# Optimization experiments

Hardware: AMD Instinct MI355X
Metric: run time of the kernel (lower is better)

## Reference

```python
import jax, jax.numpy as jnp
import numpy as np

STATE_DIM = 32
OBS_DIM = 16
PROCESS_VAR = 1e-4
MEAS_VAR = 1e-2
B = 2048
T = 64


def setup_inputs() -> dict:
    key = jax.random.key(0)
    k1, k2, k3 = jax.random.split(key, 3)
    state0 = jax.random.normal(k1, (B, STATE_DIM), dtype=jnp.float32)
    # Initial covariance P = I (per torch __init__), broadcast over batch
    cov0 = jnp.broadcast_to(jnp.eye(STATE_DIM, dtype=jnp.float32), (B, STATE_DIM, STATE_DIM))
    measurements = jax.random.normal(k2, (B, T, OBS_DIM), dtype=jnp.float32)
    # Parameters per torch __init__: F = eye, H = randn, Q = pv*I, R = mv*I
    F = jnp.eye(STATE_DIM, dtype=jnp.float32)
    H = jax.random.normal(k3, (OBS_DIM, STATE_DIM), dtype=jnp.float32)
    Q = PROCESS_VAR * jnp.eye(STATE_DIM, dtype=jnp.float32)
    R = MEAS_VAR * jnp.eye(OBS_DIM, dtype=jnp.float32)
    return {"state0": state0, "cov0": cov0, "measurements": measurements,
            "F": F, "H": H, "Q": Q, "R": R}


def reference(state0, cov0, measurements, F, H, Q, R):
    """Run Kalman predict+update over T timesteps; return filtered states (B,T,S)."""

    def step(carry, z):
        x, P = carry  # x: (B,S), P: (B,S,S); z: (B,O)
        # --- predict ---
        x_pred = x @ F.T                                   # F @ x per batch
        P_pred = jnp.einsum('ij,bjk,lk->bil', F, P, F) + Q  # F P F^T + Q
        # --- update ---
        y = x_pred @ H.T                                   # predicted measurement (B,O)
        innov = z - y
        S = jnp.einsum('ij,bjk,lk->bil', H, P_pred, H) + R  # (B,O,O)
        S_inv = jnp.linalg.inv(S)
        K = jnp.einsum('bij,kj,bkl->bil', P_pred, H, S_inv)  # P H^T S^{-1}, (B,S,O)
        x_new = x_pred + jnp.einsum('bij,bj->bi', K, innov)
        P_new = P_pred - jnp.einsum('bij,jk,bkl->bil', K, H, P_pred)  # (I - K H) P
        return (x_new, P_new), x_new

    # scan over time axis: measurements (B,T,O) -> (T,B,O)
    (_, _), states = jax.lax.scan(step, (state0, cov0), jnp.swapaxes(measurements, 0, 1))
    return jnp.swapaxes(states, 0, 1)  # (B,T,S)
```

## Files before the change

kernel.cpp:

```cpp
#include <hip/hip_runtime.h>
#include <math.h>


#define S_DIM 32
#define O_DIM 16
#define K_STRIDE 512
#define HS 36

__device__ __forceinline__ float rdlanef(float v, int srcLane) {
    return __uint_as_float(
        (unsigned int)__builtin_amdgcn_readlane((int)__float_as_uint(v), srcLane));
}

__global__ __launch_bounds__(256) void traj_kernel(
    const float* __restrict__ cov0,
    const float* __restrict__ Fm,
    const float* __restrict__ Hm,
    const float* __restrict__ Qm,
    const float* __restrict__ Rm,
    float* __restrict__ wsK,
    int T)
{
    __shared__ float P  [S_DIM*33];
    __shared__ float Fs [S_DIM*33];
    __shared__ float Qs [S_DIM*33];
    __shared__ float Tp [S_DIM*33];
    __shared__ float Hs [O_DIM*HS];
    __shared__ float HQ [O_DIM*HS];
    __shared__ float HPs[O_DIM*HS];
    __shared__ float KT [O_DIM*33];
    __shared__ float Sg [O_DIM*17];
    __shared__ float Rs [O_DIM*17];
    __shared__ int notId, notDiag, convFlag, convT;

    const int tid = threadIdx.x;

    for (int i = tid; i < S_DIM*S_DIM; i += 256) {
        int r = i >> 5, c = i & 31;
        P [r*33+c] = cov0[i];
        Fs[r*33+c] = Fm[i];
        Qs[r*33+c] = Qm[i];
    }
    for (int i = tid; i < O_DIM*S_DIM; i += 256) {
        int r = i >> 5, c = i & 31;
        Hs[r*HS+c] = Hm[i];
    }
    for (int i = tid; i < O_DIM*O_DIM; i += 256) {
        int r = i >> 4, c = i & 15;
        Rs[r*17+c] = Rm[i];
    }
    if (tid == 0) { notId = 0; notDiag = 0; convFlag = 0; convT = 0; }
    __syncthreads();

    {
        bool badI = false, badD = false;
        for (int i = tid; i < S_DIM*S_DIM; i += 256) {
            int r = i >> 5, c = i & 31;
            if (Fs[r*33+c] != ((r == c) ? 1.0f : 0.0f)) badI = true;
        }
        for (int i = tid; i < O_DIM*O_DIM; i += 256) {
            int r = i >> 4, c = i & 15;
            if (r != c && Rs[r*17+c] != 0.0f) badD = true;
        }
        if (badI) notId = 1;
        if (badD) notDiag = 1;
    }
    __syncthreads();
    const bool fId   = (notId == 0);
    const bool rDiag = (notDiag == 0);

    if (fId) {
        for (int i = tid; i < S_DIM*S_DIM; i += 256) {
            int r = i >> 5, c = i & 31;
            P[r*33+c] += Qs[r*33+c];
        }
    }
    __syncthreads();

    if (fId) {
        int i0 = tid, i1 = tid + 256;
        int r0 = i0 >> 5, c0 = i0 & 31;
        int r1 = i1 >> 5, c1 = i1 & 31;
        float a0 = 0.f, a1 = 0.f, q0 = 0.f, q1 = 0.f;
        for (int k = 0; k < S_DIM; ++k) {
            a0 += Hs[r0*HS+k]*P [k*33+c0];
            a1 += Hs[r1*HS+k]*P [k*33+c1];
            q0 += Hs[r0*HS+k]*Qs[k*33+c0];
            q1 += Hs[r1*HS+k]*Qs[k*33+c1];
        }
        HPs[r0*HS+c0] = a0;  HPs[r1*HS+c1] = a1;
        HQ [r0*HS+c0] = q0;  HQ [r1*HS+c1] = q1;
    }
    __syncthreads();

    bool  havePend = false;
    int   pendT = 0;
    float4 pf0, pf1, pf2, pf3;
    float prevK[16];

    for (int t = 0; t < T; ++t) {
        if (havePend) {
            float4* dst = (float4*)(wsK + (long)pendT*K_STRIDE + (tid - O_DIM)*O_DIM);
            dst[0] = pf0; dst[1] = pf1; dst[2] = pf2; dst[3] = pf3;
            havePend = false;
        }

        if (!fId) {
            for (int i = tid; i < S_DIM*S_DIM; i += 256) {
                int r = i >> 5, c = i & 31;
                float a = 0.f;
                for (int k = 0; k < S_DIM; ++k) a += Fs[r*33+k]*P[k*33+c];
                Tp[r*33+c] = a;
            }
            __syncthreads();
            for (int i = tid; i < S_DIM*S_DIM; i += 256) {
                int r = i >> 5, c = i & 31;
                float a = Qs[r*33+c];
                for (int k = 0; k < S_DIM; ++k) a += Tp[r*33+k]*Fs[c*33+k];
                P[r*33+c] = a;
            }
            __syncthreads();
            int i0 = tid, i1 = tid + 256;
            int r0 = i0 >> 5, c0 = i0 & 31;
            int r1 = i1 >> 5, c1 = i1 & 31;
            float a0 = 0.f, a1 = 0.f;
            for (int k = 0; k < S_DIM; ++k) {
                a0 += Hs[r0*HS+k]*P[k*33+c0];
                a1 += Hs[r1*HS+k]*P[k*33+c1];
            }
            HPs[r0*HS+c0] = a0;
            HPs[r1*HS+c1] = a1;
            __syncthreads();
        }

        {
            int r = tid >> 4, c = tid & 15;
            float a = Rs[r*17+c];
            const float4* hp = (const float4*)&HPs[r*HS];
            const float4* hh = (const float4*)&Hs [c*HS];
            #pragma unroll
            for (int k = 0; k < 8; ++k) {
                float4 u = hp[k], v = hh[k];
                a += u.x*v.x + u.y*v.y + u.z*v.z + u.w*v.w;
            }
            Sg[r*17+c] = a;
        }
        __syncthreads();

        if (tid < 64) {
            const int myc = tid;
            const bool isS = (myc < O_DIM);
            const bool isK = (!isS && myc < 48);
            const int hc = (myc - O_DIM) & 31;
            float a[16];
            #pragma unroll
            for (int r = 0; r < O_DIM; ++r)
                a[r] = isS ? Sg[r*17+myc] : HPs[r*HS+hc];

            #pragma unroll
            for (int p = 0; p < O_DIM; ++p) {
                float sp[16];
                #pragma unroll
                for (int r = 0; r < O_DIM; ++r) sp[r] = rdlanef(a[r], p);
                float pinv = __builtin_amdgcn_rcpf(sp[p]);
                float sc = a[p] * pinv;
                #pragma unroll
                for (int r = 0; r < O_DIM; ++r)
                    a[r] = (r == p) ? sc : fmaf(-sp[r], sc, a[r]);
            }

            float d = 0.f;
            if (isK) {
                #pragma unroll
                for (int r = 0; r < O_DIM; ++r) {
                    float dd = fabsf(a[r] - prevK[r]);
                    d = fmaxf(d, dd);
                    prevK[r] = a[r];
                }
            }
            unsigned long long anyBig = __ballot(isK && (d > 1e-5f));
            if (myc == 0 && anyBig == 0ull && t >= 1) {
                convFlag = 1; convT = t;
            }

            if (isK) {
                pf0 = make_float4(a[0],  a[1],  a[2],  a[3]);
                pf1 = make_float4(a[4],  a[5],  a[6],  a[7]);
                pf2 = make_float4(a[8],  a[9],  a[10], a[11]);
                pf3 = make_float4(a[12], a[13], a[14], a[15]);
                pendT = t; havePend = true;

                const int j = myc - O_DIM;
                if (fId) {
                    if (rDiag) {
                        #pragma unroll
                        for (int r = 0; r < O_DIM; ++r)
                            HPs[r*HS+j] = fmaf(Rs[r*17+r], a[r], HQ[r*HS+j]);
                    } else {
                        #pragma unroll
                        for (int r = 0; r < O_DIM; ++r) {
                            float rg = 0.f;
                            for (int k = 0; k < O_DIM; ++k) rg += Rs[r*17+k]*a[k];
                            HPs[r*HS+j] = rg + HQ[r*HS+j];
                        }
                    }
                } else {
                    #pragma unroll
                    for (int o = 0; o < O_DIM; ++o) KT[o*33+j] = a[o];
                }
            }
        }
        __syncthreads();

        if (convFlag) break;

        if (!fId) {
            for (int i = tid; i < S_DIM*S_DIM; i += 256) {
                int r = i >> 5, c = i & 31;
                float acc = 0.f;
                for (int o = 0; o < O_DIM; ++o) acc += KT[o*33+r]*HPs[o*HS+c];
                P[r*33+c] -= acc;
            }
            __syncthreads();
        }
    }

    if (havePend) {
        float4* dst = (float4*)(wsK + (long)pendT*K_STRIDE + (tid - O_DIM)*O_DIM);
        dst[0] = pf0; dst[1] = pf1; dst[2] = pf2; dst[3] = pf3;
    }
    __syncthreads();

    {
        const int tc = convFlag ? convT : (T - 1);
        const long n = (long)(T - 1 - tc) * K_STRIDE;
        const float* src = wsK + (long)tc * K_STRIDE;
        float* dst = wsK + (long)(tc + 1) * K_STRIDE;
        for (long i = tid; i < n; i += 256)
            dst[i] = src[i & (K_STRIDE - 1)];
        if (tid == 0) {
            int tailStart = (convFlag && fId) ? convT : T;
            *(int*)(wsK + (long)T * K_STRIDE) = tailStart;
        }
    }
}

__global__ __launch_bounds__(64) void batch_kernel(
    const float* __restrict__ state0,
    const float* __restrict__ meas,
    const float* __restrict__ wsK,
    const float* __restrict__ Fm,
    const float* __restrict__ Hm,
    float* __restrict__ out,
    int T)
{
    const int l = threadIdx.x;
    const int s = l & 31;
    const int h = l >> 5;
    const int o = l & 15;
    const int q = l >> 4;
    const long b = blockIdx.x;

    __shared__ float xs[32];
    __shared__ float iv[16];
    __shared__ int notId;

    const int tailStart = *(const int*)(wsK + (long)T * K_STRIDE);

    float4 h0, h1;
    {
        const float4* Hv = (const float4*)(Hm + o*S_DIM + q*8);
        h0 = Hv[0]; h1 = Hv[1];
    }

    if (l == 0) notId = 0;
    __syncthreads();
    {
        bool bad = false;
        for (int i = l; i < S_DIM*S_DIM; i += 64) {
            int r = i >> 5, c = i & 31;
            if (Fm[i] != ((r == c) ? 1.0f : 0.0f)) bad = true;
        }
        if (bad) notId = 1;
    }
    __syncthreads();
    const bool fId = (notId == 0);

    float4 f0, f1, f2, f3;
    if (!fId) {
        const float4* Fv = (const float4*)(Fm + s*S_DIM + h*16);
        f0 = Fv[0]; f1 = Fv[1]; f2 = Fv[2]; f3 = Fv[3];
    }

    float x = state0[b*S_DIM + s];
    if (h == 0) xs[s] = x;
    __syncthreads();

    float4 ka0, ka1, kb0, kb1; float za, zb;
    {
        const float4* Kv = (const float4*)(wsK + 0*K_STRIDE + s*O_DIM + h*8);
        ka0 = Kv[0]; ka1 = Kv[1];
        za = meas[(b*T + 0)*O_DIM + o];
        const int t1 = (1 < T) ? 1 : 0;
        const float4* Kv1 = (const float4*)(wsK + (long)t1*K_STRIDE + s*O_DIM + h*8);
        kb0 = Kv1[0]; kb1 = Kv1[1];
        zb = meas[(b*T + t1)*O_DIM + o];
    }

    int t = 0;
    for (; t < tailStart; ++t) {
        float4 kc0, kc1; float zc;
        {
            const int tn = (t + 2 < T) ? (t + 2) : (T - 1);
            const float4* Kv = (const float4*)(wsK + (long)tn*K_STRIDE + s*O_DIM + h*8);
            kc0 = Kv[0]; kc1 = Kv[1];
            zc = meas[(b*T + tn)*O_DIM + o];
        }

        if (!fId) {
            const float4* xv = (const float4*)(&xs[h*16]);
            float4 xa = xv[0], xb = xv[1], xc = xv[2], xd = xv[3];
            float p = f0.x*xa.x + f0.y*xa.y + f0.z*xa.z + f0.w*xa.w
                    + f1.x*xb.x + f1.y*xb.y + f1.z*xb.z + f1.w*xb.w
                    + f2.x*xc.x + f2.y*xc.y + f2.z*xc.z + f2.w*xc.w
                    + f3.x*xd.x + f3.y*xd.y + f3.z*xd.z + f3.w*xd.w;
            x = p + __shfl_xor(p, 32, 64);
            __builtin_amdgcn_wave_barrier();
            if (h == 0) xs[s] = x;
            __builtin_amdgcn_wave_barrier();
        }

        const float4* xq = (const float4*)(&xs[q*8]);
        float4 xa = xq[0], xb = xq[1];
        float p = h0.x*xa.x + h0.y*xa.y + h0.z*xa.z + h0.w*xa.w
                + h1.x*xb.x + h1.y*xb.y + h1.z*xb.z + h1.w*xb.w;
        float p2 = p + __shfl_xor(p, 16, 64);
        float y  = p2 + __shfl_xor(p2, 32, 64);
        float innov = za - y;

        __builtin_amdgcn_wave_barrier();
        if (l < 16) iv[o] = innov;
        __builtin_amdgcn_wave_barrier();

        const float4* ivq = (const float4*)(&iv[h*8]);
        float4 va = ivq[0], vb = ivq[1];
        float xp2 = ka0.x*va.x + ka0.y*va.y + ka0.z*va.z + ka0.w*va.w
                  + ka1.x*vb.x + ka1.y*vb.y + ka1.z*vb.z + ka1.w*vb.w;
        float xnew = x + (xp2 + __shfl_xor(xp2, 32, 64));

        if (h == 0) out[(b*T + t)*S_DIM + s] = xnew;

        __builtin_amdgcn_wave_barrier();
        if (h == 0) xs[s] = xnew;
        __builtin_amdgcn_wave_barrier();

        x = xnew;
        ka0 = kb0; ka1 = kb1; za = zb;
        kb0 = kc0; kb1 = kc1; zb = zc;
    }

    if (t >= T) return;

    float mreg[16];
    float4 kc0, kc1;
    {
        const float4* Kr = (const float4*)(wsK + (long)tailStart*K_STRIDE + s*O_DIM);
        float4 kq0 = Kr[0], kq1 = Kr[1], kq2 = Kr[2], kq3 = Kr[3];
        float krow[16] = {kq0.x,kq0.y,kq0.z,kq0.w, kq1.x,kq1.y,kq1.z,kq1.w,
                          kq2.x,kq2.y,kq2.z,kq2.w, kq3.x,kq3.y,kq3.z,kq3.w};
        kc0 = h ? kq2 : kq0;
        kc1 = h ? kq3 : kq1;
        #pragma unroll
        for (int j = 0; j < 16; ++j)
            mreg[j] = (s == h*16 + j) ? 1.0f : 0.0f;
        for (int oo = 0; oo < O_DIM; ++oo) {
            const float4* Hr = (const float4*)(Hm + oo*S_DIM + h*16);
            float4 a0 = Hr[0], a1 = Hr[1], a2 = Hr[2], a3 = Hr[3];
            float k = krow[oo];
            mreg[0]  = fmaf(-k, a0.x, mreg[0]);
            mreg[1]  = fmaf(-k, a0.y, mreg[1]);
            mreg[2]  = fmaf(-k, a0.z, mreg[2]);
            mreg[3]  = fmaf(-k, a0.w, mreg[3]);
            mreg[4]  = fmaf(-k, a1.x, mreg[4]);
            mreg[5]  = fmaf(-k, a1.y, mreg[5]);
            mreg[6]  = fmaf(-k, a1.z, mreg[6]);
            mreg[7]  = fmaf(-k, a1.w, mreg[7]);
            mreg[8]  = fmaf(-k, a2.x, mreg[8]);
            mreg[9]  = fmaf(-k, a2.y, mreg[9]);
            mreg[10] = fmaf(-k, a2.z, mreg[10]);
            mreg[11] = fmaf(-k, a2.w, mreg[11]);
            mreg[12] = fmaf(-k, a3.x, mreg[12]);
            mreg[13] = fmaf(-k, a3.y, mreg[13]);
            mreg[14] = fmaf(-k, a3.z, mreg[14]);
            mreg[15] = fmaf(-k, a3.w, mreg[15]);
        }
    }

    float4 zva0, zva1, zvb0, zvb1;
    {
        const float4* Zv = (const float4*)(meas + (b*T + t)*O_DIM + h*8);
        zva0 = Zv[0]; zva1 = Zv[1];
        const int t1 = (t + 1 < T) ? (t + 1) : t;
        const float4* Zv1 = (const float4*)(meas + (b*T + t1)*O_DIM + h*8);
        zvb0 = Zv1[0]; zvb1 = Zv1[1];
    }

    for (; t < T; ++t) {
        float4 zvc0, zvc1;
        {
            const int tn = (t + 2 < T) ? (t + 2) : (T - 1);
            const float4* Zv = (const float4*)(meas + (b*T + tn)*O_DIM + h*8);
            zvc0 = Zv[0]; zvc1 = Zv[1];
        }

        const float4* xv = (const float4*)(&xs[h*16]);
        float4 xa = xv[0], xb = xv[1], xc = xv[2], xd = xv[3];
        float p = mreg[0] *xa.x + mreg[1] *xa.y + mreg[2] *xa.z + mreg[3] *xa.w
                + mreg[4] *xb.x + mreg[5] *xb.y + mreg[6] *xb.z + mreg[7] *xb.w
                + mreg[8] *xc.x + mreg[9] *xc.y + mreg[10]*xc.z + mreg[11]*xc.w
                + mreg[12]*xd.x + mreg[13]*xd.y + mreg[14]*xd.z + mreg[15]*xd.w;
        p += kc0.x*zva0.x + kc0.y*zva0.y + kc0.z*zva0.z + kc0.w*zva0.w
           + kc1.x*zva1.x + kc1.y*zva1.y + kc1.z*zva1.z + kc1.w*zva1.w;
        float xnew = p + __shfl_xor(p, 32, 64);

        if (h == 0) out[(b*T + t)*S_DIM + s] = xnew;

        __builtin_amdgcn_wave_barrier();
        if (h == 0) xs[s] = xnew;
        __builtin_amdgcn_wave_barrier();

        zva0 = zvb0; zva1 = zvb1;
        zvb0 = zvc0; zvb1 = zvc1;
    }
}

extern "C" void kernel_launch(void* const* d_in, const int* in_sizes, int n_in,
                              void* d_out, int out_size, void* d_ws, size_t ws_size,
                              hipStream_t stream) {
    const float* state0 = (const float*)d_in[0];
    const float* cov0   = (const float*)d_in[1];
    const float* meas   = (const float*)d_in[2];
    const float* Fm     = (const float*)d_in[3];
    const float* Hm     = (const float*)d_in[4];
    const float* Qm     = (const float*)d_in[5];
    const float* Rm     = (const float*)d_in[6];
    float* out  = (float*)d_out;
    float* wsK  = (float*)d_ws;

    const int B = in_sizes[0] / S_DIM;
    const int T = in_sizes[2] / (B * O_DIM);

    traj_kernel<<<dim3(1), dim3(256), 0, stream>>>(cov0, Fm, Hm, Qm, Rm, wsK, T);
    batch_kernel<<<dim3(B), dim3(64), 0, stream>>>(state0, meas, wsK, Fm, Hm, out, T);
}
```

Measured before the change: 163.9 us.

## Fuse covariance and batch kernels with a flag-based producer-consumer pipeline

Merges the single-block gain trajectory kernel and the per-batch state kernel into one launch. Block 0 computes the Kalman gains and publishes progress through an atomic control word in the workspace. The other blocks each run four batch rows as separate wavefronts and spin-wait on that word, so state updates overlap with gain computation instead of waiting for a second launch. This adds a memset, polling with sleeps, and relaxed atomic loads of the gains. It also depends on block 0 being scheduled and making progress while the consumer blocks spin.

```diff
diff --git a/kernel.cpp b/kernel.cpp
--- a/kernel.cpp
+++ b/kernel.cpp
@@ -6,21 +6,30 @@
 #define O_DIM 16
 #define K_STRIDE 512
 #define HS 36
+#define CW 4
+
+typedef unsigned int u32;
 
 __device__ __forceinline__ float rdlanef(float v, int srcLane) {
     return __uint_as_float(
         (unsigned int)__builtin_amdgcn_readlane((int)__float_as_uint(v), srcLane));
 }
 
-__global__ __launch_bounds__(256) void traj_kernel(
+__global__ __launch_bounds__(256) void fused_kernel(
+    const float* __restrict__ state0,
     const float* __restrict__ cov0,
+    const float* __restrict__ meas,
     const float* __restrict__ Fm,
     const float* __restrict__ Hm,
     const float* __restrict__ Qm,
     const float* __restrict__ Rm,
     float* __restrict__ wsK,
-    int T)
+    float* __restrict__ out,
+    int T, int B)
 {
+    u32* ctrl = (u32*)(wsK + (long)T * K_STRIDE);
+    const int tid = threadIdx.x;
+
     __shared__ float P  [S_DIM*33];
     __shared__ float Fs [S_DIM*33];
     __shared__ float Qs [S_DIM*33];
@@ -32,240 +41,236 @@
     __shared__ float Sg [O_DIM*17];
     __shared__ float Rs [O_DIM*17];
     __shared__ int notId, notDiag, convFlag, convT;
-
-    const int tid = threadIdx.x;
-
-    for (int i = tid; i < S_DIM*S_DIM; i += 256) {
-        int r = i >> 5, c = i & 31;
-        P [r*33+c] = cov0[i];
-        Fs[r*33+c] = Fm[i];
-        Qs[r*33+c] = Qm[i];
-    }
-    for (int i = tid; i < O_DIM*S_DIM; i += 256) {
-        int r = i >> 5, c = i & 31;
-        Hs[r*HS+c] = Hm[i];
-    }
-    for (int i = tid; i < O_DIM*O_DIM; i += 256) {
-        int r = i >> 4, c = i & 15;
-        Rs[r*17+c] = Rm[i];
-    }
-    if (tid == 0) { notId = 0; notDiag = 0; convFlag = 0; convT = 0; }
-    __syncthreads();
-
-    {
-        bool badI = false, badD = false;
+    __shared__ float xs[CW][32];
+    __shared__ float iv[CW][16];
+
+    if (blockIdx.x == 0) {
         for (int i = tid; i < S_DIM*S_DIM; i += 256) {
             int r = i >> 5, c = i & 31;
-            if (Fs[r*33+c] != ((r == c) ? 1.0f : 0.0f)) badI = true;
+            P [r*33+c] = cov0[i];
+            Fs[r*33+c] = Fm[i];
+            Qs[r*33+c] = Qm[i];
+        }
+        for (int i = tid; i < O_DIM*S_DIM; i += 256) {
+            int r = i >> 5, c = i & 31;
+            Hs[r*HS+c] = Hm[i];
         }
         for (int i = tid; i < O_DIM*O_DIM; i += 256) {
             int r = i >> 4, c = i & 15;
-            if (r != c && Rs[r*17+c] != 0.0f) badD = true;
-        }
-        if (badI) notId = 1;
-        if (badD) notDiag = 1;
-    }
-    __syncthreads();
-    const bool fId   = (notId == 0);
-    const bool rDiag = (notDiag == 0);
-
-    if (fId) {
-        for (int i = tid; i < S_DIM*S_DIM; i += 256) {
-            int r = i >> 5, c = i & 31;
-            P[r*33+c] += Qs[r*33+c];
-        }
-    }
-    __syncthreads();
-
-    if (fId) {
-        int i0 = tid, i1 = tid + 256;
-        int r0 = i0 >> 5, c0 = i0 & 31;
-        int r1 = i1 >> 5, c1 = i1 & 31;
-        float a0 = 0.f, a1 = 0.f, q0 = 0.f, q1 = 0.f;
-        for (int k = 0; k < S_DIM; ++k) {
-            a0 += Hs[r0*HS+k]*P [k*33+c0];
-            a1 += Hs[r1*HS+k]*P [k*33+c1];
-            q0 += Hs[r0*HS+k]*Qs[k*33+c0];
-            q1 += Hs[r1*HS+k]*Qs[k*33+c1];
-        }
-        HPs[r0*HS+c0] = a0;  HPs[r1*HS+c1] = a1;
-        HQ [r0*HS+c0] = q0;  HQ [r1*HS+c1] = q1;
-    }
-    __syncthreads();
-
-    bool  havePend = false;
-    int   pendT = 0;
-    float4 pf0, pf1, pf2, pf3;
-    float prevK[16];
-
-    for (int t = 0; t < T; ++t) {
+            Rs[r*17+c] = Rm[i];
+        }
+        if (tid == 0) { notId = 0; notDiag = 0; convFlag = 0; convT = 0; }
+        __syncthreads();
+
+        {
+            bool badI = false, badD = false;
+            for (int i = tid; i < S_DIM*S_DIM; i += 256) {
+                int r = i >> 5, c = i & 31;
+                if (Fs[r*33+c] != ((r == c) ? 1.0f : 0.0f)) badI = true;
+            }
+            for (int i = tid; i < O_DIM*O_DIM; i += 256) {
+                int r = i >> 4, c = i & 15;
+                if (r != c && Rs[r*17+c] != 0.0f) badD = true;
+            }
+            if (badI) notId = 1;
+            if (badD) notDiag = 1;
+        }
+        __syncthreads();
+        const bool fId   = (notId == 0);
+        const bool rDiag = (notDiag == 0);
+
+        if (fId) {
+            for (int i = tid; i < S_DIM*S_DIM; i += 256) {
+                int r = i >> 5, c = i & 31;
+                P[r*33+c] += Qs[r*33+c];
+            }
+        }
+        __syncthreads();
+
+        if (fId) {
+            int i0 = tid, i1 = tid + 256;
+            int r0 = i0 >> 5, c0 = i0 & 31;
+            int r1 = i1 >> 5, c1 = i1 & 31;
+            float a0 = 0.f, a1 = 0.f, q0 = 0.f, q1 = 0.f;
+            for (int k = 0; k < S_DIM; ++k) {
+                a0 += Hs[r0*HS+k]*P [k*33+c0];
+                a1 += Hs[r1*HS+k]*P [k*33+c1];
+                q0 += Hs[r0*HS+k]*Qs[k*33+c0];
+                q1 += Hs[r1*HS+k]*Qs[k*33+c1];
+            }
+            HPs[r0*HS+c0] = a0;  HPs[r1*HS+c1] = a1;
+            HQ [r0*HS+c0] = q0;  HQ [r1*HS+c1] = q1;
+        }
+        __syncthreads();
+
+        bool  havePend = false;
+        int   pendT = 0;
+        float4 pf0, pf1, pf2, pf3;
+        float prevK[16];
+
+        for (int t = 0; t < T; ++t) {
+            if (havePend) {
+                float4* dst = (float4*)(wsK + (long)pendT*K_STRIDE + (tid - O_DIM)*O_DIM);
+                dst[0] = pf0; dst[1] = pf1; dst[2] = pf2; dst[3] = pf3;
+                havePend = false;
+            }
+
+            if (!fId) {
+                for (int i = tid; i < S_DIM*S_DIM; i += 256) {
+                    int r = i >> 5, c = i & 31;
+                    float a = 0.f;
+                    for (int k = 0; k < S_DIM; ++k) a += Fs[r*33+k]*P[k*33+c];
+                    Tp[r*33+c] = a;
+                }
+                __syncthreads();
+                for (int i = tid; i < S_DIM*S_DIM; i += 256) {
+                    int r = i >> 5, c = i & 31;
+                    float a = Qs[r*33+c];
+                    for (int k = 0; k < S_DIM; ++k) a += Tp[r*33+k]*Fs[c*33+k];
+                    P[r*33+c] = a;
+                }
+                __syncthreads();
+                int i0 = tid, i1 = tid + 256;
+                int r0 = i0 >> 5, c0 = i0 & 31;
+                int r1 = i1 >> 5, c1 = i1 & 31;
+                float a0 = 0.f, a1 = 0.f;
+                for (int k = 0; k < S_DIM; ++k) {
+                    a0 += Hs[r0*HS+k]*P[k*33+c0];
+                    a1 += Hs[r1*HS+k]*P[k*33+c1];
+                }
+                HPs[r0*HS+c0] = a0;
+                HPs[r1*HS+c1] = a1;
+                __syncthreads();
+            }
+
+            {
+                int r = tid >> 4, c = tid & 15;
+                float a = Rs[r*17+c];
+                const float4* hp = (const float4*)&HPs[r*HS];
+                const float4* hh = (const float4*)&Hs [c*HS];
+                #pragma unroll
+                for (int k = 0; k < 8; ++k) {
+                    float4 u = hp[k], v = hh[k];
+                    a += u.x*v.x + u.y*v.y + u.z*v.z + u.w*v.w;
+                }
+                Sg[r*17+c] = a;
+            }
+            __syncthreads();
+
+            if (tid == 255 && t > 0)
+                __hip_atomic_store(ctrl, (u32)t, __ATOMIC_RELEASE,
+                                   __HIP_MEMORY_SCOPE_AGENT);
+
+            if (tid < 64) {
+                const int myc = tid;
+                const bool isS = (myc < O_DIM);
+                const bool isK = (!isS && myc < 48);
+                const int hc = (myc - O_DIM) & 31;
+                float a[16];
+                #pragma unroll
+                for (int r = 0; r < O_DIM; ++r)
+                    a[r] = isS ? Sg[r*17+myc] : HPs[r*HS+hc];
+
+                #pragma unroll
+                for (int p = 0; p < O_DIM; ++p) {
+                    float sp[16];
+                    #pragma unroll
+                    for (int r = 0; r < O_DIM; ++r) sp[r] = rdlanef(a[r], p);
+                    float pinv = __builtin_amdgcn_rcpf(sp[p]);
+                    float sc = a[p] * pinv;
+                    #pragma unroll
+                    for (int r = 0; r < O_DIM; ++r)
+                        a[r] = (r == p) ? sc : fmaf(-sp[r], sc, a[r]);
+                }
+
+                float d = 0.f;
+                if (isK) {
+                    #pragma unroll
+                    for (int r = 0; r < O_DIM; ++r) {
+                        float dd = fabsf(a[r] - prevK[r]);
+                        d = fmaxf(d, dd);
+                        prevK[r] = a[r];
+                    }
+                }
+                unsigned long long anyBig = __ballot(isK && (d > 1e-5f));
+                if (myc == 0 && anyBig == 0ull && t >= 1) {
+                    convFlag = 1; convT = t;
+                }
+
+                if (isK) {
+                    pf0 = make_float4(a[0],  a[1],  a[2],  a[3]);
+                    pf1 = make_float4(a[4],  a[5],  a[6],  a[7]);
+                    pf2 = make_float4(a[8],  a[9],  a[10], a[11]);
+                    pf3 = make_float4(a[12], a[13], a[14], a[15]);
+                    pendT = t; havePend = true;
+
+                    const int j = myc - O_DIM;
+                    if (fId) {
+                        if (rDiag) {
+                            #pragma unroll
+                            for (int r = 0; r < O_DIM; ++r)
+                                HPs[r*HS+j] = fmaf(Rs[r*17+r], a[r], HQ[r*HS+j]);
+                        } else {
+                            #pragma unroll
+                            for (int r = 0; r < O_DIM; ++r) {
+                                float rg = 0.f;
+                                for (int k = 0; k < O_DIM; ++k) rg += Rs[r*17+k]*a[k];
+                                HPs[r*HS+j] = rg + HQ[r*HS+j];
+                            }
+                        }
+                    } else {
+                        #pragma unroll
+                        for (int o = 0; o < O_DIM; ++o) KT[o*33+j] = a[o];
+                    }
+                }
+            }
+            __syncthreads();
+
+            if (convFlag) break;
+
+            if (!fId) {
+                for (int i = tid; i < S_DIM*S_DIM; i += 256) {
+                    int r = i >> 5, c = i & 31;
+                    float acc = 0.f;
+                    for (int o = 0; o < O_DIM; ++o) acc += KT[o*33+r]*HPs[o*HS+c];
+                    P[r*33+c] -= acc;
+                }
+                __syncthreads();
+            }
+        }
+
         if (havePend) {
             float4* dst = (float4*)(wsK + (long)pendT*K_STRIDE + (tid - O_DIM)*O_DIM);
             dst[0] = pf0; dst[1] = pf1; dst[2] = pf2; dst[3] = pf3;
-            havePend = false;
-        }
-
-        if (!fId) {
-            for (int i = tid; i < S_DIM*S_DIM; i += 256) {
-                int r = i >> 5, c = i & 31;
-                float a = 0.f;
-                for (int k = 0; k < S_DIM; ++k) a += Fs[r*33+k]*P[k*33+c];
-                Tp[r*33+c] = a;
-            }
+        }
+        __syncthreads();
+
+        if (!fId && convFlag) {
+            const int tc = convT;
+            const long n = (long)(T - 1 - tc) * K_STRIDE;
+            const float* src = wsK + (long)tc * K_STRIDE;
+            float* dst = wsK + (long)(tc + 1) * K_STRIDE;
+            for (long i = tid; i < n; i += 256)
+                dst[i] = src[i & (K_STRIDE - 1)];
             __syncthreads();
-            for (int i = tid; i < S_DIM*S_DIM; i += 256) {
-                int r = i >> 5, c = i & 31;
-                float a = Qs[r*33+c];
-                for (int k = 0; k < S_DIM; ++k) a += Tp[r*33+k]*Fs[c*33+k];
-                P[r*33+c] = a;
-            }
-            __syncthreads();
-            int i0 = tid, i1 = tid + 256;
-            int r0 = i0 >> 5, c0 = i0 & 31;
-            int r1 = i1 >> 5, c1 = i1 & 31;
-            float a0 = 0.f, a1 = 0.f;
-            for (int k = 0; k < S_DIM; ++k) {
-                a0 += Hs[r0*HS+k]*P[k*33+c0];
-                a1 += Hs[r1*HS+k]*P[k*33+c1];
-            }
-            HPs[r0*HS+c0] = a0;
-            HPs[r1*HS+c1] = a1;
-            __syncthreads();
-        }
-
-        {
-            int r = tid >> 4, c = tid & 15;
-            float a = Rs[r*17+c];
-            const float4* hp = (const float4*)&HPs[r*HS];
-            const float4* hh = (const float4*)&Hs [c*HS];
-            #pragma unroll
-            for (int k = 0; k < 8; ++k) {
-                float4 u = hp[k], v = hh[k];
-                a += u.x*v.x + u.y*v.y + u.z*v.z + u.w*v.w;
-            }
-            Sg[r*17+c] = a;
-        }
-        __syncthreads();
-
-        if (tid < 64) {
-            const int myc = tid;
-            const bool isS = (myc < O_DIM);
-            const bool isK = (!isS && myc < 48);
-            const int hc = (myc - O_DIM) & 31;
-            float a[16];
-            #pragma unroll
-            for (int r = 0; r < O_DIM; ++r)
-                a[r] = isS ? Sg[r*17+myc] : HPs[r*HS+hc];
-
-            #pragma unroll
-            for (int p = 0; p < O_DIM; ++p) {
-                float sp[16];
-                #pragma unroll
-                for (int r = 0; r < O_DIM; ++r) sp[r] = rdlanef(a[r], p);
-                float pinv = __builtin_amdgcn_rcpf(sp[p]);
-                float sc = a[p] * pinv;
-                #pragma unroll
-                for (int r = 0; r < O_DIM; ++r)
-                    a[r] = (r == p) ? sc : fmaf(-sp[r], sc, a[r]);
-            }
-
-            float d = 0.f;
-            if (isK) {
-                #pragma unroll
-                for (int r = 0; r < O_DIM; ++r) {
-                    float dd = fabsf(a[r] - prevK[r]);
-                    d = fmaxf(d, dd);
-                    prevK[r] = a[r];
-                }
-            }
-            unsigned long long anyBig = __ballot(isK && (d > 1e-5f));
-            if (myc == 0 && anyBig == 0ull && t >= 1) {
-                convFlag = 1; convT = t;
-            }
-
-            if (isK) {
-                pf0 = make_float4(a[0],  a[1],  a[2],  a[3]);
-                pf1 = make_float4(a[4],  a[5],  a[6],  a[7]);
-                pf2 = make_float4(a[8],  a[9],  a[10], a[11]);
-                pf3 = make_float4(a[12], a[13], a[14], a[15]);
-                pendT = t; havePend = true;
-
-                const int j = myc - O_DIM;
-                if (fId) {
-                    if (rDiag) {
-                        #pragma unroll
-                        for (int r = 0; r < O_DIM; ++r)
-                            HPs[r*HS+j] = fmaf(Rs[r*17+r], a[r], HQ[r*HS+j]);
-                    } else {
-                        #pragma unroll
-                        for (int r = 0; r < O_DIM; ++r) {
-                            float rg = 0.f;
-                            for (int k = 0; k < O_DIM; ++k) rg += Rs[r*17+k]*a[k];
-                            HPs[r*HS+j] = rg + HQ[r*HS+j];
-                        }
-                    }
-                } else {
-                    #pragma unroll
-                    for (int o = 0; o < O_DIM; ++o) KT[o*33+j] = a[o];
-                }
-            }
-        }
-        __syncthreads();
-
-        if (convFlag) break;
-
-        if (!fId) {
-            for (int i = tid; i < S_DIM*S_DIM; i += 256) {
-                int r = i >> 5, c = i & 31;
-                float acc = 0.f;
-                for (int o = 0; o < O_DIM; ++o) acc += KT[o*33+r]*HPs[o*HS+c];
-                P[r*33+c] -= acc;
-            }
-            __syncthreads();
-        }
-    }
-
-    if (havePend) {
-        float4* dst = (float4*)(wsK + (long)pendT*K_STRIDE + (tid - O_DIM)*O_DIM);
-        dst[0] = pf0; dst[1] = pf1; dst[2] = pf2; dst[3] = pf3;
-    }
-    __syncthreads();
-
-    {
-        const int tc = convFlag ? convT : (T - 1);
-        const long n = (long)(T - 1 - tc) * K_STRIDE;
-        const float* src = wsK + (long)tc * K_STRIDE;
-        float* dst = wsK + (long)(tc + 1) * K_STRIDE;
-        for (long i = tid; i < n; i += 256)
-            dst[i] = src[i & (K_STRIDE - 1)];
+        }
+
         if (tid == 0) {
-            int tailStart = (convFlag && fId) ? convT : T;
-            *(int*)(wsK + (long)T * K_STRIDE) = tailStart;
-        }
-    }
-}
-
-__global__ __launch_bounds__(64) void batch_kernel(
-    const float* __restrict__ state0,
-    const float* __restrict__ meas,
-    const float* __restrict__ wsK,
-    const float* __restrict__ Fm,
-    const float* __restrict__ Hm,
-    float* __restrict__ out,
-    int T)
-{
-    const int l = threadIdx.x;
+            u32 tsv = (convFlag && fId) ? (u32)convT : (u32)T;
+            __hip_atomic_store(ctrl, (tsv << 16) | (u32)T, __ATOMIC_RELEASE,
+                               __HIP_MEMORY_SCOPE_AGENT);
+        }
+        return;
+    }
+
+    const int wv = tid >> 6;
+    const int l  = tid & 63;
     const int s = l & 31;
     const int h = l >> 5;
     const int o = l & 15;
     const int q = l >> 4;
-    const long b = blockIdx.x;
-
-    __shared__ float xs[32];
-    __shared__ float iv[16];
-    __shared__ int notId;
-
-    const int tailStart = *(const int*)(wsK + (long)T * K_STRIDE);
+    const long b = (long)(blockIdx.x - 1) * CW + wv;
+    if (b >= B) return;
 
     float4 h0, h1;
     {
@@ -273,18 +278,12 @@
         h0 = Hv[0]; h1 = Hv[1];
     }
 
-    if (l == 0) notId = 0;
-    __syncthreads();
-    {
-        bool bad = false;
-        for (int i = l; i < S_DIM*S_DIM; i += 64) {
-            int r = i >> 5, c = i & 31;
-            if (Fm[i] != ((r == c) ? 1.0f : 0.0f)) bad = true;
-        }
-        if (bad) notId = 1;
-    }
-    __syncthreads();
-    const bool fId = (notId == 0);
+    bool bad = false;
+    for (int i = l; i < S_DIM*S_DIM; i += 64) {
+        int r = i >> 5, c = i & 31;
+        if (Fm[i] != ((r == c) ? 1.0f : 0.0f)) bad = true;
+    }
+    const bool fId = !__any(bad);
 
     float4 f0, f1, f2, f3;
     if (!fId) {
@@ -293,32 +292,38 @@
     }
 
     float x = state0[b*S_DIM + s];
-    if (h == 0) xs[s] = x;
-    __syncthreads();
-
-    float4 ka0, ka1, kb0, kb1; float za, zb;
-    {
-        const float4* Kv = (const float4*)(wsK + 0*K_STRIDE + s*O_DIM + h*8);
-        ka0 = Kv[0]; ka1 = Kv[1];
-        za = meas[(b*T + 0)*O_DIM + o];
-        const int t1 = (1 < T) ? 1 : 0;
-        const float4* Kv1 = (const float4*)(wsK + (long)t1*K_STRIDE + s*O_DIM + h*8);
-        kb0 = Kv1[0]; kb1 = Kv1[1];
-        zb = meas[(b*T + t1)*O_DIM + o];
-    }
-
+    if (h == 0) xs[wv][s] = x;
+    __builtin_amdgcn_wave_barrier();
+
+    int avail = 0, ts = 0;
     int t = 0;
-    for (; t < tailStart; ++t) {
-        float4 kc0, kc1; float zc;
-        {
-            const int tn = (t + 2 < T) ? (t + 2) : (T - 1);
-            const float4* Kv = (const float4*)(wsK + (long)tn*K_STRIDE + s*O_DIM + h*8);
-            kc0 = Kv[0]; kc1 = Kv[1];
-            zc = meas[(b*T + tn)*O_DIM + o];
-        }
+    bool toTail = false;
+
+    for (; t < T; ++t) {
+        if (ts != 0 && t >= ts) { toTail = true; break; }
+        while (avail <= t) {
+            u32 cw = __hip_atomic_load(ctrl, __ATOMIC_RELAXED,
+                                       __HIP_MEMORY_SCOPE_AGENT);
+            avail = (int)(cw & 0xFFFFu);
+            ts    = (int)(cw >> 16);
+            if (ts != 0 && t >= ts) { toTail = true; break; }
+            if (avail <= t) __builtin_amdgcn_s_sleep(4);
+        }
+        if (toTail) break;
+
+        const float* Kp = wsK + (long)t*K_STRIDE + s*O_DIM + h*8;
+        float k0 = __hip_atomic_load(Kp+0, __ATOMIC_RELAXED, __HIP_MEMORY_SCOPE_AGENT);
+        float k1 = __hip_atomic_load(Kp+1, __ATOMIC_RELAXED, __HIP_MEMORY_SCOPE_AGENT);
+        float k2 = __hip_atomic_load(Kp+2, __ATOMIC_RELAXED, __HIP_MEMORY_SCOPE_AGENT);
+        float k3 = __hip_atomic_load(Kp+3, __ATOMIC_RELAXED, __HIP_MEMORY_SCOPE_AGENT);
+        float k4 = __hip_atomic_load(Kp+4, __ATOMIC_RELAXED, __HIP_MEMORY_SCOPE_AGENT);
+        float k5 = __hip_atomic_load(Kp+5, __ATOMIC_RELAXED, __HIP_MEMORY_SCOPE_AGENT);
+        float k6 = __hip_atomic_load(Kp+6, __ATOMIC_RELAXED, __HIP_MEMORY_SCOPE_AGENT);
+        float k7 = __hip_atomic_load(Kp+7, __ATOMIC_RELAXED, __HIP_MEMORY_SCOPE_AGENT);
+        float za = meas[(b*T + t)*O_DIM + o];
 
         if (!fId) {
-            const float4* xv = (const float4*)(&xs[h*16]);
+            const float4* xv = (const float4*)(&xs[wv][h*16]);
             float4 xa = xv[0], xb = xv[1], xc = xv[2], xd = xv[3];
             float p = f0.x*xa.x + f0.y*xa.y + f0.z*xa.z + f0.w*xa.w
                     + f1.x*xb.x + f1.y*xb.y + f1.z*xb.z + f1.w*xb.w
@@ -326,11 +331,11 @@
                     + f3.x*xd.x + f3.y*xd.y + f3.z*xd.z + f3.w*xd.w;
             x = p + __shfl_xor(p, 32, 64);
             __builtin_amdgcn_wave_barrier();
-            if (h == 0) xs[s] = x;
+            if (h == 0) xs[wv][s] = x;
             __builtin_amdgcn_wave_barrier();
         }
 
-        const float4* xq = (const float4*)(&xs[q*8]);
+        const float4* xq = (const float4*)(&xs[wv][q*8]);
         float4 xa = xq[0], xb = xq[1];
         float p = h0.x*xa.x + h0.y*xa.y + h0.z*xa.z + h0.w*xa.w
                 + h1.x*xb.x + h1.y*xb.y + h1.z*xb.z + h1.w*xb.w;
@@ -339,61 +344,64 @@
         float innov = za - y;
 
         __builtin_amdgcn_wave_barrier();
-        if (l < 16) iv[o] = innov;
-        __builtin_amdgcn_wave_barrier();
-
-        const float4* ivq = (const float4*)(&iv[h*8]);
+        if (l < 16) iv[wv][o] = innov;
+        __builtin_amdgcn_wave_barrier();
+
+        const float4* ivq = (const float4*)(&iv[wv][h*8]);
         float4 va = ivq[0], vb = ivq[1];
-        float xp2 = ka0.x*va.x + ka0.y*va.y + ka0.z*va.z + ka0.w*va.w
-                  + ka1.x*vb.x + ka1.y*vb.y + ka1.z*vb.z + ka1.w*vb.w;
+        float xp2 = k0*va.x + k1*va.y + k2*va.z + k3*va.w
+                  + k4*vb.x + k5*vb.y + k6*vb.z + k7*vb.w;
         float xnew = x + (xp2 + __shfl_xor(xp2, 32, 64));
 
         if (h == 0) out[(b*T + t)*S_DIM + s] = xnew;
 
         __builtin_amdgcn_wave_barrier();
-        if (h == 0) xs[s] = xnew;
+        if (h == 0) xs[wv][s] = xnew;
         __builtin_amdgcn_wave_barrier();
 
         x = xnew;
-        ka0 = kb0; ka1 = kb1; za = zb;
-        kb0 = kc0; kb1 = kc1; zb = zc;
-    }
-
-    if (t >= T) return;
-
-    float mreg[16];
-    float4 kc0, kc1;
+    }
+
+    if (!toTail) return;
+
+    float ka[16];
     {
-        const float4* Kr = (const float4*)(wsK + (long)tailStart*K_STRIDE + s*O_DIM);
-        float4 kq0 = Kr[0], kq1 = Kr[1], kq2 = Kr[2], kq3 = Kr[3];
-        float krow[16] = {kq0.x,kq0.y,kq0.z,kq0.w, kq1.x,kq1.y,kq1.z,kq1.w,
-                          kq2.x,kq2.y,kq2.z,kq2.w, kq3.x,kq3.y,kq3.z,kq3.w};
-        kc0 = h ? kq2 : kq0;
-        kc1 = h ? kq3 : kq1;
+        const float* Kr = wsK + (long)ts*K_STRIDE + s*O_DIM;
         #pragma unroll
         for (int j = 0; j < 16; ++j)
-            mreg[j] = (s == h*16 + j) ? 1.0f : 0.0f;
-        for (int oo = 0; oo < O_DIM; ++oo) {
-            const float4* Hr = (const float4*)(Hm + oo*S_DIM + h*16);
-            float4 a0 = Hr[0], a1 = Hr[1], a2 = Hr[2], a3 = Hr[3];
-            float k = krow[oo];
-            mreg[0]  = fmaf(-k, a0.x, mreg[0]);
-            mreg[1]  = fmaf(-k, a0.y, mreg[1]);
-            mreg[2]  = fmaf(-k, a0.z, mreg[2]);
-            mreg[3]  = fmaf(-k, a0.w, mreg[3]);
-            mreg[4]  = fmaf(-k, a1.x, mreg[4]);
-            mreg[5]  = fmaf(-k, a1.y, mreg[5]);
-            mreg[6]  = fmaf(-k, a1.z, mreg[6]);
-            mreg[7]  = fmaf(-k, a1.w, mreg[7]);
-            mreg[8]  = fmaf(-k, a2.x, mreg[8]);
-            mreg[9]  = fmaf(-k, a2.y, mreg[9]);
-            mreg[10] = fmaf(-k, a2.z, mreg[10]);
-            mreg[11] = fmaf(-k, a2.w, mreg[11]);
-            mreg[12] = fmaf(-k, a3.x, mreg[12]);
-            mreg[13] = fmaf(-k, a3.y, mreg[13]);
-            mreg[14] = fmaf(-k, a3.z, mreg[14]);
-            mreg[15] = fmaf(-k, a3.w, mreg[15]);
-        }
+            ka[j] = __hip_atomic_load(Kr + j, __ATOMIC_RELAXED,
+                                      __HIP_MEMORY_SCOPE_AGENT);
+    }
+    float4 kc0, kc1;
+    kc0.x = h ? ka[8]  : ka[0];  kc0.y = h ? ka[9]  : ka[1];
+    kc0.z = h ? ka[10] : ka[2];  kc0.w = h ? ka[11] : ka[3];
+    kc1.x = h ? ka[12] : ka[4];  kc1.y = h ? ka[13] : ka[5];
+    kc1.z = h ? ka[14] : ka[6];  kc1.w = h ? ka[15] : ka[7];
+
+    float mreg[16];
+    #pragma unroll
+    for (int j = 0; j < 16; ++j)
+        mreg[j] = (s == h*16 + j) ? 1.0f : 0.0f;
+    for (int oo = 0; oo < O_DIM; ++oo) {
+        const float4* Hr = (const float4*)(Hm + oo*S_DIM + h*16);
+        float4 a0 = Hr[0], a1 = Hr[1], a2 = Hr[2], a3 = Hr[3];
+        float k = ka[oo];
+        mreg[0]  = fmaf(-k, a0.x, mreg[0]);
+        mreg[1]  = fmaf(-k, a0.y, mreg[1]);
+        mreg[2]  = fmaf(-k, a0.z, mreg[2]);
+        mreg[3]  = fmaf(-k, a0.w, mreg[3]);
+        mreg[4]  = fmaf(-k, a1.x, mreg[4]);
+        mreg[5]  = fmaf(-k, a1.y, mreg[5]);
+        mreg[6]  = fmaf(-k, a1.z, mreg[6]);
+        mreg[7]  = fmaf(-k, a1.w, mreg[7]);
+        mreg[8]  = fmaf(-k, a2.x, mreg[8]);
+        mreg[9]  = fmaf(-k, a2.y, mreg[9]);
+        mreg[10] = fmaf(-k, a2.z, mreg[10]);
+        mreg[11] = fmaf(-k, a2.w, mreg[11]);
+        mreg[12] = fmaf(-k, a3.x, mreg[12]);
+        mreg[13] = fmaf(-k, a3.y, mreg[13]);
+        mreg[14] = fmaf(-k, a3.z, mreg[14]);
+        mreg[15] = fmaf(-k, a3.w, mreg[15]);
     }
 
     float4 zva0, zva1, zvb0, zvb1;
@@ -413,7 +421,7 @@
             zvc0 = Zv[0]; zvc1 = Zv[1];
         }
 
-        const float4* xv = (const float4*)(&xs[h*16]);
+        const float4* xv = (const float4*)(&xs[wv][h*16]);
         float4 xa = xv[0], xb = xv[1], xc = xv[2], xd = xv[3];
         float p = mreg[0] *xa.x + mreg[1] *xa.y + mreg[2] *xa.z + mreg[3] *xa.w
                 + mreg[4] *xb.x + mreg[5] *xb.y + mreg[6] *xb.z + mreg[7] *xb.w
@@ -426,7 +434,7 @@
         if (h == 0) out[(b*T + t)*S_DIM + s] = xnew;
 
         __builtin_amdgcn_wave_barrier();
-        if (h == 0) xs[s] = xnew;
+        if (h == 0) xs[wv][s] = xnew;
         __builtin_amdgcn_wave_barrier();
 
         zva0 = zvb0; zva1 = zvb1;
@@ -450,6 +458,9 @@
     const int B = in_sizes[0] / S_DIM;
     const int T = in_sizes[2] / (B * O_DIM);
 
-    traj_kernel<<<dim3(1), dim3(256), 0, stream>>>(cov0, Fm, Hm, Qm, Rm, wsK, T);
-    batch_kernel<<<dim3(B), dim3(64), 0, stream>>>(state0, meas, wsK, Fm, Hm, out, T);
+    hipMemsetAsync((void*)(wsK + (long)T * K_STRIDE), 0, sizeof(unsigned int), stream);
+
+    const int grid = 1 + (B + CW - 1) / CW;
+    fused_kernel<<<dim3(grid), dim3(256), 0, stream>>>(
+        state0, cov0, meas, Fm, Hm, Qm, Rm, wsK, out, T, B);
 }
```

After: 154.5 us. 5.8% less time.
